# Kernel tuning notes

Hardware: AMD Instinct MI355X
Metric: run time of the kernel (lower is better)

The kernel has to match this reference:

```python
import jax, jax.numpy as jnp
import numpy as np

PAD, SOS, EOS = 0, 2, 3
B, S, T = 32, 64, 32
E, HE, HD = 300, 256, 512
VE, VD = 50000, 50000

def _p(k, shape, s=0.05):
    return jax.random.normal(k, shape, dtype=jnp.float32) * s

def setup_inputs():
    ks = jax.random.split(jax.random.key(0), 22)
    return dict(
        data=jax.random.randint(ks[0], (B, S), 0, VE),
        target=jax.random.randint(ks[1], (B, T), 0, VD),
        data_len=jnp.full((B,), S, dtype=jnp.int32),
        target_len=jnp.full((B,), T, dtype=jnp.int32),
        emb_enc=_p(ks[2], (VE, E)).at[PAD].set(0.0),
        emb_dec=_p(ks[3], (VD, E)).at[PAD].set(0.0),
        Wihf=_p(ks[4], (3 * HE, E)), Whhf=_p(ks[5], (3 * HE, HE)),
        bihf=_p(ks[6], (3 * HE,)), bhhf=_p(ks[7], (3 * HE,)),
        Wihb=_p(ks[8], (3 * HE, E)), Whhb=_p(ks[9], (3 * HE, HE)),
        bihb=_p(ks[10], (3 * HE,)), bhhb=_p(ks[11], (3 * HE,)),
        Wihd=_p(ks[12], (3 * HD, E + 2 * HE)), Whhd=_p(ks[13], (3 * HD, HD)),
        bihd=_p(ks[14], (3 * HD,)), bhhd=_p(ks[15], (3 * HD,)),
        Wattn=_p(ks[16], (2 * HE, HD + E)), battn=_p(ks[17], (2 * HE,)),
        Wout=_p(ks[18], (VD, HD)), bout=_p(ks[19], (VD,)),
    )

def gru_cell(x, h, W_ih, W_hh, b_ih, b_hh):
    # PyTorch GRU cell: gates ordered (r, z, n)
    gi = x @ W_ih.T + b_ih
    gh = h @ W_hh.T + b_hh
    i_r, i_z, i_n = jnp.split(gi, 3, axis=-1)
    h_r, h_z, h_n = jnp.split(gh, 3, axis=-1)
    r = jax.nn.sigmoid(i_r + h_r)
    z = jax.nn.sigmoid(i_z + h_z)
    n = jnp.tanh(i_n + r * h_n)
    return (1.0 - z) * n + z * h

def _forward(data, target, emb_enc, emb_dec, Wihf, Whhf, bihf, bhhf,
             Wihb, Whhb, bihb, bhhb, Wihd, Whhd, bihd, bhhd,
             Wattn, battn, Wout, bout):
    # ---- bidirectional 1-layer GRU encoder ----
    x = emb_enc[data]                          # [B,S,E] (dropout p=0 -> identity)
    xt = jnp.swapaxes(x, 0, 1)                 # [S,B,E]
    h0 = jnp.zeros((data.shape[0], HE), dtype=x.dtype)
    def stepf(h, xi):
        h2 = gru_cell(xi, h, Wihf, Whhf, bihf, bhhf)
        return h2, h2
    def stepb(h, xi):
        h2 = gru_cell(xi, h, Wihb, Whhb, bihb, bhhb)
        return h2, h2
    hf, yf = jax.lax.scan(stepf, h0, xt)
    hb, yb = jax.lax.scan(stepb, h0, xt[::-1])
    enc_out = jnp.swapaxes(jnp.concatenate([yf, yb[::-1]], axis=-1), 0, 1)  # [B,S,2HE]
    h_dec = jnp.concatenate([hf, hb], axis=-1)                              # [B,HD]

    # ---- greedy attention decoder loop (teacher_forcing_ratio=0.0) ----
    inp0 = jnp.full((data.shape[0],), SOS, dtype=jnp.int32)
    def dec_step(carry, _):
        h, inp = carry
        emb = emb_dec[inp]                                        # [B,E]
        q = jnp.concatenate([emb, h], axis=-1) @ Wattn.T + battn  # [B,2HE]
        scores = jnp.einsum('bd,bsd->bs', q, enc_out)             # [B,S]
        aw = jax.nn.softmax(scores, axis=-1)
        ctx = jnp.einsum('bs,bsd->bd', aw, enc_out)               # [B,2HE]
        h2 = gru_cell(jnp.concatenate([emb, ctx], axis=-1), h, Wihd, Whhd, bihd, bhhd)
        logp = jax.nn.log_softmax(h2 @ Wout.T + bout, axis=-1)    # [B,VD]
        nxt = jnp.argmax(logp, axis=-1).astype(jnp.int32)         # topk(1), detached
        return (h2, nxt), (logp, nxt, aw)
    _, (logps, idxs, aws) = jax.lax.scan(dec_step, (h_dec, inp0), None, length=T)
    decoder_output = jnp.swapaxes(logps, 0, 1)   # [B,T,VD]
    decoder_idx = jnp.swapaxes(idxs, 0, 1)       # [B,T]
    att_weights = jnp.swapaxes(aws, 0, 1)        # [B,T,S]
    # mask[i, j:] = 0 from the first EOS (inclusive)
    mask = (jnp.cumsum((decoder_idx == EOS).astype(jnp.int32), axis=1) == 0).astype(jnp.float32)
    return decoder_output, decoder_idx, mask, att_weights

def reference(data, target, data_len, target_len, emb_enc, emb_dec,
              Wihf, Whhf, bihf, bhhf, Wihb, Whhb, bihb, bhhb,
              Wihd, Whhd, bihd, bhhd, Wattn, battn, Wout, bout):
    return _forward(data, target, emb_enc, emb_dec, Wihf, Whhf, bihf, bhhf,
                    Wihb, Whhb, bihb, bhhb, Wihd, Whhd, bihd, bhhd,
                    Wattn, battn, Wout, bout)
```

## Files before the change

kernel.cpp:

```cpp
#include <hip/hip_runtime.h>
#include <stdint.h>

#define B 32
#define S 64
#define T 32
#define E 300
#define HE 256
#define HD 512
#define VD 50000
#define GE 768
#define GD 1536
#define CATN 812
#define SOS 2
#define EOS 3

#define SZ_WIHT3   (E*HE*3)
#define SZ_WHHT3   (HE*HE*3)
#define SZ_WATTNT4 (CATN*HD)
#define SZ_WIHDT3  (CATN*HD*3)
#define SZ_WHHDT3  (HD*HD*3)
#define SZ_GI      (S*B*HE*3)
#define SZ_ENCOUT  (B*S*HD)

constexpr size_t OFF_WIHT3F  = 0;
constexpr size_t OFF_WIHT3B  = OFF_WIHT3F + SZ_WIHT3 + 4;
constexpr size_t OFF_WHHT3F  = OFF_WIHT3B + SZ_WIHT3 + 4;
constexpr size_t OFF_WHHT3B  = OFF_WHHT3F + SZ_WHHT3 + 4;
constexpr size_t OFF_WATTNT4 = OFF_WHHT3B + SZ_WHHT3 + 4;
constexpr size_t OFF_WIHDT3  = OFF_WATTNT4 + SZ_WATTNT4;
constexpr size_t OFF_WHHDT3  = OFF_WIHDT3 + SZ_WIHDT3 + 4;
constexpr size_t OFF_GIF     = OFF_WHHDT3 + SZ_WHHDT3 + 4;
constexpr size_t OFF_GIB     = OFF_GIF + SZ_GI + 4;
constexpr size_t OFF_ENCOUT  = OFF_GIB + SZ_GI + 4;
constexpr size_t OFF_HBUF    = OFF_ENCOUT + SZ_ENCOUT;
constexpr size_t OFF_QBUF    = OFF_HBUF + B*HD;
constexpr size_t OFF_GHBUF   = OFF_QBUF + B*HD;
constexpr size_t OFF_GIEBUF  = OFF_GHBUF + 3*B*HD;
constexpr size_t OFF_CTXBUF  = OFF_GIEBUF + 3*B*HD;
constexpr size_t OFF_EXPSUM  = OFF_CTXBUF + B*HD;
constexpr size_t OFF_LSE     = OFF_EXPSUM + T*B;
constexpr size_t OFF_PACKED  = OFF_LSE + T*B;

constexpr size_t O_IDX  = (size_t)B*T*VD;
constexpr size_t O_MASK = O_IDX + B*T;
constexpr size_t O_ATT  = O_MASK + B*T;

struct __align__(4) f4u { float x, y, z, w; };
__device__ __forceinline__ f4u ld4u(const float* p) { return *(const f4u*)p; }

__device__ __forceinline__ float sigm(float x) { return 1.0f / (1.0f + __expf(-x)); }
__device__ __forceinline__ float tanhfast(float x) {
    float e = __expf(2.0f * fminf(x, 15.0f));
    return (e - 1.0f) / (e + 1.0f);
}

__global__ __launch_bounds__(256) void k_prep(
    const float* __restrict__ Wihf, const float* __restrict__ Whhf,
    const float* __restrict__ Wihb, const float* __restrict__ Whhb,
    const float* __restrict__ Wihd, const float* __restrict__ Whhd,
    const float* __restrict__ Wattn, float* __restrict__ ws)
{
    const size_t NWIH = (size_t)GE * E;
    const size_t NWHH = (size_t)GE * HE;
    const size_t NATT = (size_t)HD * CATN;
    const size_t NWID = (size_t)GD * CATN;
    const size_t NWHD = (size_t)GD * HD;
    size_t i = (size_t)blockIdx.x * 256 + threadIdx.x;

    if (i < 2 * NWIH) {
        int d = i >= NWIH;
        size_t r = i - (d ? NWIH : 0);
        int row = (int)(r / E), k = (int)(r - (size_t)row * E);
        int g = row >> 8, j = row & 255;
        const float* src = d ? Wihb : Wihf;
        ws[(d ? OFF_WIHT3B : OFF_WIHT3F) + ((size_t)k * HE + j) * 3 + g] = src[r];
        return;
    }
    i -= 2 * NWIH;
    if (i < 2 * NWHH) {
        int d = i >= NWHH;
        size_t r = i - (d ? NWHH : 0);
        int row = (int)(r / HE), k = (int)(r & (HE - 1));
        int g = row >> 8, j = row & 255;
        const float* src = d ? Whhb : Whhf;
        ws[(d ? OFF_WHHT3B : OFF_WHHT3F) + ((size_t)k * HE + j) * 3 + g] = src[r];
        return;
    }
    i -= 2 * NWHH;
    if (i < NATT) {
        int row = (int)(i / CATN), k = (int)(i - (size_t)row * CATN);
        ws[OFF_WATTNT4 + (((size_t)(k >> 2) * HD + row) << 2) + (k & 3)] = Wattn[i];
        return;
    }
    i -= NATT;
    if (i < NWID) {
        int row = (int)(i / CATN), k = (int)(i - (size_t)row * CATN);
        int g = row >> 9, j = row & 511;
        ws[OFF_WIHDT3 + ((size_t)k * HD + j) * 3 + g] = Wihd[i];
        return;
    }
    i -= NWID;
    if (i < NWHD) {
        int row = (int)(i / HD), k = (int)(i & (HD - 1));
        int g = row >> 9, j = row & 511;
        ws[OFF_WHHDT3 + ((size_t)k * HD + j) * 3 + g] = Whhd[i];
        return;
    }
    i -= NWHD;
    if (i < 4096) ws[OFF_EXPSUM + i] = 0.0f;
}

__global__ __launch_bounds__(256) void k_enc_gi(
    const int* __restrict__ data, const float* __restrict__ emb_enc,
    const float* __restrict__ bihf, const float* __restrict__ bihb,
    float* __restrict__ ws)
{
    int s = blockIdx.x, dir = blockIdx.y, b0 = blockIdx.z * 16;
    int tid = threadIdx.x;
    __shared__ float xT[E * 16];
    int s_eff = dir ? (S - 1 - s) : s;
    for (int idx = tid; idx < 16 * E; idx += 256) {
        int bb = idx / E, k = idx - bb * E;
        int tok = data[(b0 + bb) * S + s_eff];
        xT[k * 16 + bb] = emb_enc[(size_t)tok * E + k];
    }
    __syncthreads();
    const float* W3 = ws + (dir ? OFF_WIHT3B : OFF_WIHT3F);
    const float* bih = dir ? bihb : bihf;
    int j = tid;
    float aR[16], aZ[16], aN[16];
#pragma unroll
    for (int bb = 0; bb < 16; bb++) { aR[bb] = 0.f; aZ[bb] = 0.f; aN[bb] = 0.f; }
    for (int k = 0; k < E; k++) {
        f4u w = ld4u(W3 + ((size_t)k * HE + j) * 3);
        const float* xk = &xT[k * 16];
#pragma unroll
        for (int bb = 0; bb < 16; bb++) {
            float x = xk[bb];
            aR[bb] += x * w.x; aZ[bb] += x * w.y; aN[bb] += x * w.z;
        }
    }
    float br = bih[j], bz = bih[HE + j], bn = bih[2 * HE + j];
    float* gi = ws + (dir ? OFF_GIB : OFF_GIF);
#pragma unroll
    for (int bb = 0; bb < 16; bb++) {
        size_t base = (((size_t)s * B + b0 + bb) * HE + j) * 3;
        gi[base + 0] = aR[bb] + br;
        gi[base + 1] = aZ[bb] + bz;
        gi[base + 2] = aN[bb] + bn;
    }
}

__global__ __launch_bounds__(1024) void k_enc_rec(
    const float* __restrict__ bhhf, const float* __restrict__ bhhb,
    float* __restrict__ ws)
{
    int b = blockIdx.x, dir = blockIdx.y;
    int tid = threadIdx.x;
    int j = tid & 255, kc = tid >> 8;
    __shared__ float h[2][HE];
    __shared__ float part[3][4][HE];
    if (tid < HE) h[0][tid] = 0.f;
    __syncthreads();
    const float* W3 = ws + (dir ? OFF_WHHT3B : OFF_WHHT3F);
    const float* gi = ws + (dir ? OFF_GIB : OFF_GIF);
    const float* bhh = dir ? bhhb : bhhf;
    float* enc = ws + OFF_ENCOUT;
    float br = bhh[j], bz = bhh[HE + j], bn = bhh[2 * HE + j];
    const float* Wp = W3 + ((size_t)(kc * 64) * HE + j) * 3;
    for (int s = 0; s < S; s++) {
        const float* hc = h[s & 1];
        float gr = 0.f, gz = 0.f, gn = 0.f;
#pragma unroll 4
        for (int k4 = 0; k4 < 16; k4++) {
            float4 h4 = *(const float4*)&hc[kc * 64 + k4 * 4];
#pragma unroll
            for (int kk = 0; kk < 4; kk++) {
                f4u w = ld4u(Wp + ((size_t)(k4 * 4 + kk) * HE) * 3);
                float hv = (kk == 0) ? h4.x : (kk == 1) ? h4.y : (kk == 2) ? h4.z : h4.w;
                gr += hv * w.x; gz += hv * w.y; gn += hv * w.z;
            }
        }
        part[0][kc][j] = gr; part[1][kc][j] = gz; part[2][kc][j] = gn;
        __syncthreads();
        if (kc == 0) {
            float sgr = part[0][0][j] + part[0][1][j] + part[0][2][j] + part[0][3][j] + br;
            float sgz = part[1][0][j] + part[1][1][j] + part[1][2][j] + part[1][3][j] + bz;
            float sgn = part[2][0][j] + part[2][1][j] + part[2][2][j] + part[2][3][j] + bn;
            f4u g = ld4u(gi + (((size_t)s * B + b) * HE + j) * 3);
            float hold = hc[j];
            float r = sigm(g.x + sgr);
            float z = sigm(g.y + sgz);
            float n = tanhfast(g.z + r * sgn);
            float hn = (1.f - z) * n + z * hold;
            h[(s + 1) & 1][j] = hn;
            int s_store = dir ? (S - 1 - s) : s;
            enc[((size_t)b * S + s_store) * HD + dir * HE + j] = hn;
            if (s == S - 1) ws[OFF_HBUF + (size_t)b * HD + dir * HE + j] = hn;
        }
        __syncthreads();
    }
}

__device__ __forceinline__ int decode_inp(const float* ws, int t, int b) {
    if (t == 0) return SOS;
    const unsigned long long* pm = (const unsigned long long*)(ws + OFF_PACKED);
    unsigned long long p = pm[(size_t)(t - 1) * B + b];
    return (VD - 1) - (int)(unsigned)(p & 0xffffffffu);
}

__global__ __launch_bounds__(256) void k_dec1(
    const float* __restrict__ emb_dec, const float* __restrict__ battn,
    const float* __restrict__ bhhd, const float* __restrict__ bihd,
    float* __restrict__ ws, int t)
{
    int jc = blockIdx.x, bg = blockIdx.y, kind = blockIdx.z;
    int tid = threadIdx.x;
    int jl = tid & 31, bb8 = tid >> 5;
    int b0 = bg * 8;
    __shared__ float cat[8][816];
    for (int bb = 0; bb < 8; bb++) {
        int inp = decode_inp(ws, t, b0 + bb);
        const float* eb = emb_dec + (size_t)inp * E;
        const float* hb = ws + OFF_HBUF + (size_t)(b0 + bb) * HD;
        for (int k = tid; k < CATN; k += 256)
            cat[bb][k] = (k < E) ? eb[k] : hb[k - E];
    }
    __syncthreads();
    int j = jc * 32 + jl;
    int b = b0 + bb8;
    if (kind == 0) {
        float acc = battn[j];
        const float* W4 = ws + OFF_WATTNT4;
        for (int k4 = 0; k4 < CATN / 4; k4++) {
            float4 c4 = *(const float4*)&cat[bb8][k4 * 4];
            float4 w4 = *(const float4*)&W4[((size_t)k4 * HD + j) << 2];
            acc += c4.x * w4.x + c4.y * w4.y + c4.z * w4.z + c4.w * w4.w;
        }
        ws[OFF_QBUF + (size_t)b * HD + j] = acc;
    } else if (kind == 1) {
        float gr = bhhd[j], gz = bhhd[HD + j], gn = bhhd[2 * HD + j];
        const float* W3 = ws + OFF_WHHDT3;
        for (int k4 = 0; k4 < HD / 4; k4++) {
            float4 h4 = *(const float4*)&cat[bb8][E + k4 * 4];
#pragma unroll
            for (int kk = 0; kk < 4; kk++) {
                f4u w = ld4u(W3 + ((size_t)(k4 * 4 + kk) * HD + j) * 3);
                float hv = (kk == 0) ? h4.x : (kk == 1) ? h4.y : (kk == 2) ? h4.z : h4.w;
                gr += hv * w.x; gz += hv * w.y; gn += hv * w.z;
            }
        }
        float* gh = ws + OFF_GHBUF;
        gh[0 * B * HD + (size_t)b * HD + j] = gr;
        gh[1 * B * HD + (size_t)b * HD + j] = gz;
        gh[2 * B * HD + (size_t)b * HD + j] = gn;
    } else {
        float gr = bihd[j], gz = bihd[HD + j], gn = bihd[2 * HD + j];
        const float* W3 = ws + OFF_WIHDT3;
        for (int k4 = 0; k4 < E / 4; k4++) {
            float4 x4 = *(const float4*)&cat[bb8][k4 * 4];
#pragma unroll
            for (int kk = 0; kk < 4; kk++) {
                f4u w = ld4u(W3 + ((size_t)(k4 * 4 + kk) * HD + j) * 3);
                float xv = (kk == 0) ? x4.x : (kk == 1) ? x4.y : (kk == 2) ? x4.z : x4.w;
                gr += xv * w.x; gz += xv * w.y; gn += xv * w.z;
            }
        }
        float* ge = ws + OFF_GIEBUF;
        ge[0 * B * HD + (size_t)b * HD + j] = gr;
        ge[1 * B * HD + (size_t)b * HD + j] = gz;
        ge[2 * B * HD + (size_t)b * HD + j] = gn;
    }
}

__global__ __launch_bounds__(256) void k_dec_attn(
    float* __restrict__ ws, float* __restrict__ out, int t)
{
    int b = blockIdx.x, tid = threadIdx.x;
    __shared__ float q[HD];
    __shared__ float awl[S];
    const float* qb = ws + OFF_QBUF + (size_t)b * HD;
    for (int k = tid; k < HD; k += 256) q[k] = qb[k];
    __syncthreads();
    if (tid < S) {
        int s = tid;
        const float* enc = ws + OFF_ENCOUT + ((size_t)b * S + s) * HD;
        float sc = 0.f;
        for (int k4 = 0; k4 < HD / 4; k4++) {
            float4 q4 = *(const float4*)&q[k4 * 4];
            float4 e4 = *(const float4*)&enc[k4 * 4];
            sc += q4.x * e4.x + q4.y * e4.y + q4.z * e4.z + q4.w * e4.w;
        }
        float m = sc;
        for (int off = 32; off; off >>= 1) m = fmaxf(m, __shfl_xor(m, off));
        float e = __expf(sc - m);
        float sum = e;
        for (int off = 32; off; off >>= 1) sum += __shfl_xor(sum, off);
        float aw = e / sum;
        out[O_ATT + ((size_t)b * T + t) * S + s] = aw;
        awl[s] = aw;
    }
    __syncthreads();
    const float* encb = ws + OFF_ENCOUT + (size_t)b * S * HD;
    float* ctx = ws + OFF_CTXBUF + (size_t)b * HD;
    for (int jj = 0; jj < HD / 256; jj++) {
        int jIdx = jj * 256 + tid;
        float acc = 0.f;
        for (int ss = 0; ss < S; ss++) acc += awl[ss] * encb[(size_t)ss * HD + jIdx];
        ctx[jIdx] = acc;
    }
}

__global__ __launch_bounds__(256) void k_dec3(float* __restrict__ ws, int t)
{
    int jc = blockIdx.x, bg = blockIdx.y;
    int tid = threadIdx.x;
    int jl = tid & 31, bb = tid >> 5;
    int j = jc * 32 + jl, b = bg * 8 + bb;
    __shared__ float xc[8 * HD];
    for (int idx = tid; idx < 8 * HD; idx += 256) {
        int bbb = idx >> 9, k = idx & 511;
        xc[idx] = ws[OFF_CTXBUF + (size_t)(bg * 8 + bbb) * HD + k];
    }
    __syncthreads();
    const float* W3 = ws + OFF_WIHDT3;
    float gr = ws[OFF_GIEBUF + 0 * B * HD + (size_t)b * HD + j];
    float gz = ws[OFF_GIEBUF + 1 * B * HD + (size_t)b * HD + j];
    float gn = ws[OFF_GIEBUF + 2 * B * HD + (size_t)b * HD + j];
    const float* xrow = &xc[bb * HD];
    for (int k4 = 0; k4 < HD / 4; k4++) {
        float4 x4 = *(const float4*)&xrow[k4 * 4];
#pragma unroll
        for (int kk = 0; kk < 4; kk++) {
            f4u w = ld4u(W3 + ((size_t)(E + k4 * 4 + kk) * HD + j) * 3);
            float xv = (kk == 0) ? x4.x : (kk == 1) ? x4.y : (kk == 2) ? x4.z : x4.w;
            gr += xv * w.x; gz += xv * w.y; gn += xv * w.z;
        }
    }
    float ghr = ws[OFF_GHBUF + 0 * B * HD + (size_t)b * HD + j];
    float ghz = ws[OFF_GHBUF + 1 * B * HD + (size_t)b * HD + j];
    float ghn = ws[OFF_GHBUF + 2 * B * HD + (size_t)b * HD + j];
    float hold = ws[OFF_HBUF + (size_t)b * HD + j];
    float r = sigm(gr + ghr);
    float z = sigm(gz + ghz);
    float n = tanhfast(gn + r * ghn);
    ws[OFF_HBUF + (size_t)b * HD + j] = (1.f - z) * n + z * hold;
}

__global__ __launch_bounds__(256) void k_proj(
    const float* __restrict__ Wout, const float* __restrict__ bout,
    float* __restrict__ ws, float* __restrict__ out, int t)
{
    int v = blockIdx.x * 256 + threadIdx.x;
    int b0 = blockIdx.y * 8;
    bool valid = v < VD;
    __shared__ float hl[8 * HD];
    __shared__ float red_e[4][8];
    __shared__ unsigned long long red_m[4][8];
    const float* hb = ws + OFF_HBUF;
    for (int idx = threadIdx.x; idx < 8 * HD; idx += 256)
        hl[idx] = hb[(size_t)(b0 + (idx >> 9)) * HD + (idx & 511)];
    __syncthreads();

    float acc[8];
    float bo = valid ? bout[v] : 0.f;
#pragma unroll
    for (int bb = 0; bb < 8; bb++) acc[bb] = bo;
    const float* wrow = Wout + (size_t)(valid ? v : 0) * HD;
    for (int k4 = 0; k4 < HD / 4; k4++) {
        float4 w4 = *(const float4*)&wrow[k4 * 4];
#pragma unroll
        for (int bb = 0; bb < 8; bb++) {
            float4 h4 = *(const float4*)&hl[bb * HD + k4 * 4];
            acc[bb] = fmaf(w4.x, h4.x, fmaf(w4.y, h4.y,
                      fmaf(w4.z, h4.z, fmaf(w4.w, h4.w, acc[bb]))));
        }
    }
    if (valid) {
#pragma unroll
        for (int bb = 0; bb < 8; bb++)
            out[((size_t)(b0 + bb) * T + t) * VD + v] = acc[bb];
    }
    int wv = threadIdx.x >> 6, lane = threadIdx.x & 63;
#pragma unroll
    for (int bb = 0; bb < 8; bb++) {
        float val = valid ? acc[bb] : -__builtin_inff();
        unsigned u = __float_as_uint(val);
        u = (u & 0x80000000u) ? ~u : (u | 0x80000000u);
        unsigned long long pk =
            ((unsigned long long)u << 32) | (unsigned)(valid ? (VD - 1 - v) : 0);
        float e = valid ? __expf(acc[bb]) : 0.f;
        for (int off = 32; off; off >>= 1) {
            unsigned long long o = __shfl_xor(pk, off);
            pk = (o > pk) ? o : pk;
            e += __shfl_xor(e, off);
        }
        if (lane == 0) { red_e[wv][bb] = e; red_m[wv][bb] = pk; }
    }
    __syncthreads();
    if (threadIdx.x < 8) {
        int bb = threadIdx.x;
        float e = red_e[0][bb] + red_e[1][bb] + red_e[2][bb] + red_e[3][bb];
        unsigned long long pk = red_m[0][bb];
        pk = red_m[1][bb] > pk ? red_m[1][bb] : pk;
        pk = red_m[2][bb] > pk ? red_m[2][bb] : pk;
        pk = red_m[3][bb] > pk ? red_m[3][bb] : pk;
        atomicAdd(ws + OFF_EXPSUM + (size_t)t * B + b0 + bb, e);
        atomicMax((unsigned long long*)(ws + OFF_PACKED) + (size_t)t * B + b0 + bb, pk);
    }
}

__global__ void k_fin_small(float* __restrict__ ws, float* __restrict__ out)
{
    int b = threadIdx.x;
    if (b >= B) return;
    const unsigned long long* pmax = (const unsigned long long*)(ws + OFF_PACKED);
    int eos = 0;
    for (int t = 0; t < T; t++) {
        unsigned long long p = pmax[(size_t)t * B + b];
        int v = (VD - 1) - (int)(unsigned)(p & 0xffffffffu);
        out[O_IDX + (size_t)b * T + t] = (float)v;
        if (v == EOS) eos++;
        out[O_MASK + (size_t)b * T + t] = (eos == 0) ? 1.f : 0.f;
        ws[OFF_LSE + (size_t)t * B + b] = logf(ws[OFF_EXPSUM + (size_t)t * B + b]);
    }
}

__global__ __launch_bounds__(256) void k_logp(
    const float* __restrict__ ws, float* __restrict__ out)
{
    size_t gid = (size_t)blockIdx.x * 256 + threadIdx.x;
    const size_t NQ = (size_t)B * T * (VD / 4);
    if (gid >= NQ) return;
    size_t row = gid / (VD / 4);
    int c4 = (int)(gid - row * (VD / 4));
    int b = (int)(row >> 5), t = (int)(row & 31);
    float L = ws[OFF_LSE + (size_t)t * B + b];
    float4* p = (float4*)(out + row * VD + (size_t)c4 * 4);
    float4 x = *p;
    x.x -= L; x.y -= L; x.z -= L; x.w -= L;
    *p = x;
}

extern "C" void kernel_launch(void* const* d_in, const int* in_sizes, int n_in,
                              void* d_out, int out_size, void* d_ws, size_t ws_size,
                              hipStream_t stream)
{
    (void)in_sizes; (void)n_in; (void)out_size; (void)ws_size;
    const int*   data    = (const int*)d_in[0];
    const float* emb_enc = (const float*)d_in[4];
    const float* emb_dec = (const float*)d_in[5];
    const float* Wihf    = (const float*)d_in[6];
    const float* Whhf    = (const float*)d_in[7];
    const float* bihf    = (const float*)d_in[8];
    const float* bhhf    = (const float*)d_in[9];
    const float* Wihb    = (const float*)d_in[10];
    const float* Whhb    = (const float*)d_in[11];
    const float* bihb    = (const float*)d_in[12];
    const float* bhhb    = (const float*)d_in[13];
    const float* Wihd    = (const float*)d_in[14];
    const float* Whhd    = (const float*)d_in[15];
    const float* bihd    = (const float*)d_in[16];
    const float* bhhd    = (const float*)d_in[17];
    const float* Wattn   = (const float*)d_in[18];
    const float* battn   = (const float*)d_in[19];
    const float* Wout    = (const float*)d_in[20];
    const float* bout    = (const float*)d_in[21];
    float* ws  = (float*)d_ws;
    float* out = (float*)d_out;

    k_prep<<<dim3(12920), dim3(256), 0, stream>>>(Wihf, Whhf, Wihb, Whhb,
                                                  Wihd, Whhd, Wattn, ws);
    k_enc_gi<<<dim3(S, 2, 2), dim3(256), 0, stream>>>(data, emb_enc, bihf, bihb, ws);
    k_enc_rec<<<dim3(B, 2), dim3(1024), 0, stream>>>(bhhf, bhhb, ws);

    for (int t = 0; t < T; t++) {
        k_dec1<<<dim3(16, 4, 3), dim3(256), 0, stream>>>(emb_dec, battn, bhhd, bihd, ws, t);
        k_dec_attn<<<dim3(B), dim3(256), 0, stream>>>(ws, out, t);
        k_dec3<<<dim3(16, 4), dim3(256), 0, stream>>>(ws, t);
        k_proj<<<dim3((VD + 255) / 256, 4), dim3(256), 0, stream>>>(Wout, bout, ws, out, t);
    }
    k_fin_small<<<dim3(1), dim3(64), 0, stream>>>(ws, out);
    k_logp<<<dim3((B * T * (VD / 4) + 255) / 256), dim3(256), 0, stream>>>(ws, out);
}
```

Before: 7.998 ms.

## Transpose Wout for coalesced projection, batch encoder recurrence, fuse decoder GRU kernels

Adds a one-time transpose of Wout into the workspace so the per-step vocabulary projection reads coalesced columns, and widens each projection block to 16 batch rows so every weight read is reused more. The encoder recurrence now processes 4 batch rows per block, reusing each weight load across them. The decoder's three-way kernel and the context GRU kernel are restructured into a query kernel and one fused GRU kernel, with a double-buffered hidden state. Attention scores move to a wave-parallel dot product. The cost is an extra transpose pass and workspace for a 100MB copy of Wout, plus higher register pressure in the projection.

```diff
diff --git a/kernel.cpp b/kernel.cpp
--- a/kernel.cpp
+++ b/kernel.cpp
@@ -33,13 +33,12 @@
 constexpr size_t OFF_GIB     = OFF_GIF + SZ_GI + 4;
 constexpr size_t OFF_ENCOUT  = OFF_GIB + SZ_GI + 4;
 constexpr size_t OFF_HBUF    = OFF_ENCOUT + SZ_ENCOUT;
-constexpr size_t OFF_QBUF    = OFF_HBUF + B*HD;
-constexpr size_t OFF_GHBUF   = OFF_QBUF + B*HD;
-constexpr size_t OFF_GIEBUF  = OFF_GHBUF + 3*B*HD;
-constexpr size_t OFF_CTXBUF  = OFF_GIEBUF + 3*B*HD;
+constexpr size_t OFF_QBUF    = OFF_HBUF + 2*B*HD;
+constexpr size_t OFF_CTXBUF  = OFF_QBUF + B*HD;
 constexpr size_t OFF_EXPSUM  = OFF_CTXBUF + B*HD;
 constexpr size_t OFF_LSE     = OFF_EXPSUM + T*B;
 constexpr size_t OFF_PACKED  = OFF_LSE + T*B;
+constexpr size_t OFF_WOUTT   = OFF_PACKED + 2*T*B;
 
 constexpr size_t O_IDX  = (size_t)B*T*VD;
 constexpr size_t O_MASK = O_IDX + B*T;
@@ -110,6 +109,28 @@
     if (i < 4096) ws[OFF_EXPSUM + i] = 0.0f;
 }
 
+__global__ __launch_bounds__(256) void k_transp(
+    const float* __restrict__ Wout, float* __restrict__ ws)
+{
+    __shared__ float tile[64][65];
+    int k0 = blockIdx.x * 64, v0 = blockIdx.y * 64;
+    int c = threadIdx.x & 63, r0 = threadIdx.x >> 6;
+#pragma unroll
+    for (int rr = 0; rr < 16; rr++) {
+        int r = r0 * 16 + rr;
+        int v = v0 + r;
+        tile[r][c] = (v < VD) ? Wout[(size_t)v * HD + k0 + c] : 0.f;
+    }
+    __syncthreads();
+    float* WT = ws + OFF_WOUTT;
+#pragma unroll
+    for (int rr = 0; rr < 16; rr++) {
+        int r = r0 * 16 + rr;
+        int v = v0 + c;
+        if (v < VD) WT[(size_t)(k0 + r) * VD + v] = tile[c][r];
+    }
+}
+
 __global__ __launch_bounds__(256) void k_enc_gi(
     const int* __restrict__ data, const float* __restrict__ emb_enc,
     const float* __restrict__ bihf, const float* __restrict__ bihb,
@@ -155,12 +176,12 @@
     const float* __restrict__ bhhf, const float* __restrict__ bhhb,
     float* __restrict__ ws)
 {
-    int b = blockIdx.x, dir = blockIdx.y;
+    int b0 = blockIdx.x * 4, dir = blockIdx.y;
     int tid = threadIdx.x;
     int j = tid & 255, kc = tid >> 8;
-    __shared__ float h[2][HE];
-    __shared__ float part[3][4][HE];
-    if (tid < HE) h[0][tid] = 0.f;
+    __shared__ float h[2][4][HE];
+    __shared__ float part[4][4][3][HE];
+    h[0][tid >> 8][tid & 255] = 0.f;
     __syncthreads();
     const float* W3 = ws + (dir ? OFF_WHHT3B : OFF_WHHT3F);
     const float* gi = ws + (dir ? OFF_GIB : OFF_GIF);
@@ -169,34 +190,49 @@
     float br = bhh[j], bz = bhh[HE + j], bn = bhh[2 * HE + j];
     const float* Wp = W3 + ((size_t)(kc * 64) * HE + j) * 3;
     for (int s = 0; s < S; s++) {
-        const float* hc = h[s & 1];
-        float gr = 0.f, gz = 0.f, gn = 0.f;
-#pragma unroll 4
+        int cur = s & 1, nxt = cur ^ 1;
+        float ar[4], az[4], an[4];
+#pragma unroll
+        for (int bb = 0; bb < 4; bb++) { ar[bb] = 0.f; az[bb] = 0.f; an[bb] = 0.f; }
+#pragma unroll 2
         for (int k4 = 0; k4 < 16; k4++) {
-            float4 h4 = *(const float4*)&hc[kc * 64 + k4 * 4];
+            float4 h4[4];
+#pragma unroll
+            for (int bb = 0; bb < 4; bb++)
+                h4[bb] = *(const float4*)&h[cur][bb][kc * 64 + k4 * 4];
 #pragma unroll
             for (int kk = 0; kk < 4; kk++) {
                 f4u w = ld4u(Wp + ((size_t)(k4 * 4 + kk) * HE) * 3);
-                float hv = (kk == 0) ? h4.x : (kk == 1) ? h4.y : (kk == 2) ? h4.z : h4.w;
-                gr += hv * w.x; gz += hv * w.y; gn += hv * w.z;
+#pragma unroll
+                for (int bb = 0; bb < 4; bb++) {
+                    float hv = (kk == 0) ? h4[bb].x : (kk == 1) ? h4[bb].y
+                             : (kk == 2) ? h4[bb].z : h4[bb].w;
+                    ar[bb] += hv * w.x; az[bb] += hv * w.y; an[bb] += hv * w.z;
+                }
             }
         }
-        part[0][kc][j] = gr; part[1][kc][j] = gz; part[2][kc][j] = gn;
+#pragma unroll
+        for (int bb = 0; bb < 4; bb++) {
+            part[kc][bb][0][j] = ar[bb];
+            part[kc][bb][1][j] = az[bb];
+            part[kc][bb][2][j] = an[bb];
+        }
         __syncthreads();
-        if (kc == 0) {
-            float sgr = part[0][0][j] + part[0][1][j] + part[0][2][j] + part[0][3][j] + br;
-            float sgz = part[1][0][j] + part[1][1][j] + part[1][2][j] + part[1][3][j] + bz;
-            float sgn = part[2][0][j] + part[2][1][j] + part[2][2][j] + part[2][3][j] + bn;
-            f4u g = ld4u(gi + (((size_t)s * B + b) * HE + j) * 3);
-            float hold = hc[j];
+        {
+            int bb = kc;
+            float sgr = part[0][bb][0][j] + part[1][bb][0][j] + part[2][bb][0][j] + part[3][bb][0][j] + br;
+            float sgz = part[0][bb][1][j] + part[1][bb][1][j] + part[2][bb][1][j] + part[3][bb][1][j] + bz;
+            float sgn = part[0][bb][2][j] + part[1][bb][2][j] + part[2][bb][2][j] + part[3][bb][2][j] + bn;
+            f4u g = ld4u(gi + (((size_t)s * B + b0 + bb) * HE + j) * 3);
+            float hold = h[cur][bb][j];
             float r = sigm(g.x + sgr);
             float z = sigm(g.y + sgz);
             float n = tanhfast(g.z + r * sgn);
             float hn = (1.f - z) * n + z * hold;
-            h[(s + 1) & 1][j] = hn;
+            h[nxt][bb][j] = hn;
             int s_store = dir ? (S - 1 - s) : s;
-            enc[((size_t)b * S + s_store) * HD + dir * HE + j] = hn;
-            if (s == S - 1) ws[OFF_HBUF + (size_t)b * HD + dir * HE + j] = hn;
+            enc[((size_t)(b0 + bb) * S + s_store) * HD + dir * HE + j] = hn;
+            if (s == S - 1) ws[OFF_HBUF + (size_t)(b0 + bb) * HD + dir * HE + j] = hn;
         }
         __syncthreads();
     }
@@ -209,181 +245,181 @@
     return (VD - 1) - (int)(unsigned)(p & 0xffffffffu);
 }
 
-__global__ __launch_bounds__(256) void k_dec1(
+__global__ __launch_bounds__(256) void k_dq(
     const float* __restrict__ emb_dec, const float* __restrict__ battn,
-    const float* __restrict__ bhhd, const float* __restrict__ bihd,
     float* __restrict__ ws, int t)
 {
-    int jc = blockIdx.x, bg = blockIdx.y, kind = blockIdx.z;
+    int jc = blockIdx.x, b0 = blockIdx.y * 8;
     int tid = threadIdx.x;
     int jl = tid & 31, bb8 = tid >> 5;
-    int b0 = bg * 8;
+    const float* hcur = ws + OFF_HBUF + (size_t)(t & 1) * B * HD;
     __shared__ float cat[8][816];
     for (int bb = 0; bb < 8; bb++) {
         int inp = decode_inp(ws, t, b0 + bb);
         const float* eb = emb_dec + (size_t)inp * E;
-        const float* hb = ws + OFF_HBUF + (size_t)(b0 + bb) * HD;
+        const float* hb = hcur + (size_t)(b0 + bb) * HD;
         for (int k = tid; k < CATN; k += 256)
             cat[bb][k] = (k < E) ? eb[k] : hb[k - E];
     }
     __syncthreads();
-    int j = jc * 32 + jl;
-    int b = b0 + bb8;
-    if (kind == 0) {
-        float acc = battn[j];
-        const float* W4 = ws + OFF_WATTNT4;
-        for (int k4 = 0; k4 < CATN / 4; k4++) {
-            float4 c4 = *(const float4*)&cat[bb8][k4 * 4];
-            float4 w4 = *(const float4*)&W4[((size_t)k4 * HD + j) << 2];
-            acc += c4.x * w4.x + c4.y * w4.y + c4.z * w4.z + c4.w * w4.w;
-        }
-        ws[OFF_QBUF + (size_t)b * HD + j] = acc;
-    } else if (kind == 1) {
-        float gr = bhhd[j], gz = bhhd[HD + j], gn = bhhd[2 * HD + j];
-        const float* W3 = ws + OFF_WHHDT3;
-        for (int k4 = 0; k4 < HD / 4; k4++) {
-            float4 h4 = *(const float4*)&cat[bb8][E + k4 * 4];
-#pragma unroll
-            for (int kk = 0; kk < 4; kk++) {
-                f4u w = ld4u(W3 + ((size_t)(k4 * 4 + kk) * HD + j) * 3);
-                float hv = (kk == 0) ? h4.x : (kk == 1) ? h4.y : (kk == 2) ? h4.z : h4.w;
-                gr += hv * w.x; gz += hv * w.y; gn += hv * w.z;
-            }
-        }
-        float* gh = ws + OFF_GHBUF;
-        gh[0 * B * HD + (size_t)b * HD + j] = gr;
-        gh[1 * B * HD + (size_t)b * HD + j] = gz;
-        gh[2 * B * HD + (size_t)b * HD + j] = gn;
-    } else {
-        float gr = bihd[j], gz = bihd[HD + j], gn = bihd[2 * HD + j];
-        const float* W3 = ws + OFF_WIHDT3;
-        for (int k4 = 0; k4 < E / 4; k4++) {
-            float4 x4 = *(const float4*)&cat[bb8][k4 * 4];
-#pragma unroll
-            for (int kk = 0; kk < 4; kk++) {
-                f4u w = ld4u(W3 + ((size_t)(k4 * 4 + kk) * HD + j) * 3);
-                float xv = (kk == 0) ? x4.x : (kk == 1) ? x4.y : (kk == 2) ? x4.z : x4.w;
-                gr += xv * w.x; gz += xv * w.y; gn += xv * w.z;
-            }
-        }
-        float* ge = ws + OFF_GIEBUF;
-        ge[0 * B * HD + (size_t)b * HD + j] = gr;
-        ge[1 * B * HD + (size_t)b * HD + j] = gz;
-        ge[2 * B * HD + (size_t)b * HD + j] = gn;
-    }
-}
-
-__global__ __launch_bounds__(256) void k_dec_attn(
+    int j = jc * 32 + jl, b = b0 + bb8;
+    float acc = battn[j];
+    const float* W4 = ws + OFF_WATTNT4;
+    for (int k4 = 0; k4 < CATN / 4; k4++) {
+        float4 c4 = *(const float4*)&cat[bb8][k4 * 4];
+        float4 w4 = *(const float4*)&W4[((size_t)k4 * HD + j) << 2];
+        acc += c4.x * w4.x + c4.y * w4.y + c4.z * w4.z + c4.w * w4.w;
+    }
+    ws[OFF_QBUF + (size_t)b * HD + j] = acc;
+}
+
+__global__ __launch_bounds__(256) void k_attn(
     float* __restrict__ ws, float* __restrict__ out, int t)
 {
     int b = blockIdx.x, tid = threadIdx.x;
+    int wv = tid >> 6, lane = tid & 63;
     __shared__ float q[HD];
+    __shared__ float scs[S];
     __shared__ float awl[S];
     const float* qb = ws + OFF_QBUF + (size_t)b * HD;
     for (int k = tid; k < HD; k += 256) q[k] = qb[k];
     __syncthreads();
-    if (tid < S) {
-        int s = tid;
-        const float* enc = ws + OFF_ENCOUT + ((size_t)b * S + s) * HD;
-        float sc = 0.f;
-        for (int k4 = 0; k4 < HD / 4; k4++) {
-            float4 q4 = *(const float4*)&q[k4 * 4];
-            float4 e4 = *(const float4*)&enc[k4 * 4];
-            sc += q4.x * e4.x + q4.y * e4.y + q4.z * e4.z + q4.w * e4.w;
-        }
-        float m = sc;
+    const float* encb = ws + OFF_ENCOUT + (size_t)b * S * HD;
+    float4 qa = *(const float4*)&q[lane * 4];
+    float4 qb4 = *(const float4*)&q[256 + lane * 4];
+#pragma unroll 4
+    for (int i = 0; i < 16; i++) {
+        int s = wv * 16 + i;
+        const float* e = encb + (size_t)s * HD;
+        float4 ea = *(const float4*)&e[lane * 4];
+        float4 eb = *(const float4*)&e[256 + lane * 4];
+        float p = ea.x * qa.x + ea.y * qa.y + ea.z * qa.z + ea.w * qa.w
+                + eb.x * qb4.x + eb.y * qb4.y + eb.z * qb4.z + eb.w * qb4.w;
+        for (int off = 32; off; off >>= 1) p += __shfl_xor(p, off);
+        if (lane == 0) scs[s] = p;
+    }
+    __syncthreads();
+    if (tid < 64) {
+        float v = scs[tid];
+        float m = v;
         for (int off = 32; off; off >>= 1) m = fmaxf(m, __shfl_xor(m, off));
-        float e = __expf(sc - m);
+        float e = __expf(v - m);
         float sum = e;
         for (int off = 32; off; off >>= 1) sum += __shfl_xor(sum, off);
         float aw = e / sum;
-        out[O_ATT + ((size_t)b * T + t) * S + s] = aw;
-        awl[s] = aw;
-    }
-    __syncthreads();
-    const float* encb = ws + OFF_ENCOUT + (size_t)b * S * HD;
+        awl[tid] = aw;
+        out[O_ATT + ((size_t)b * T + t) * S + tid] = aw;
+    }
+    __syncthreads();
     float* ctx = ws + OFF_CTXBUF + (size_t)b * HD;
-    for (int jj = 0; jj < HD / 256; jj++) {
-        int jIdx = jj * 256 + tid;
+    for (int j = tid; j < HD; j += 256) {
         float acc = 0.f;
-        for (int ss = 0; ss < S; ss++) acc += awl[ss] * encb[(size_t)ss * HD + jIdx];
-        ctx[jIdx] = acc;
-    }
-}
-
-__global__ __launch_bounds__(256) void k_dec3(float* __restrict__ ws, int t)
-{
-    int jc = blockIdx.x, bg = blockIdx.y;
+        for (int ss = 0; ss < S; ss++) acc += awl[ss] * encb[(size_t)ss * HD + j];
+        ctx[j] = acc;
+    }
+}
+
+__global__ __launch_bounds__(256) void k_dgru(
+    const float* __restrict__ emb_dec,
+    const float* __restrict__ bihd, const float* __restrict__ bhhd,
+    float* __restrict__ ws, int t)
+{
+    int jc = blockIdx.x, b0 = blockIdx.y * 8;
     int tid = threadIdx.x;
-    int jl = tid & 31, bb = tid >> 5;
-    int j = jc * 32 + jl, b = bg * 8 + bb;
-    __shared__ float xc[8 * HD];
-    for (int idx = tid; idx < 8 * HD; idx += 256) {
-        int bbb = idx >> 9, k = idx & 511;
-        xc[idx] = ws[OFF_CTXBUF + (size_t)(bg * 8 + bbb) * HD + k];
-    }
-    __syncthreads();
-    const float* W3 = ws + OFF_WIHDT3;
-    float gr = ws[OFF_GIEBUF + 0 * B * HD + (size_t)b * HD + j];
-    float gz = ws[OFF_GIEBUF + 1 * B * HD + (size_t)b * HD + j];
-    float gn = ws[OFF_GIEBUF + 2 * B * HD + (size_t)b * HD + j];
-    const float* xrow = &xc[bb * HD];
-    for (int k4 = 0; k4 < HD / 4; k4++) {
-        float4 x4 = *(const float4*)&xrow[k4 * 4];
+    int jl = tid & 31, bb8 = tid >> 5;
+    const float* hcur = ws + OFF_HBUF + (size_t)(t & 1) * B * HD;
+    float* hnxt = ws + OFF_HBUF + (size_t)((t + 1) & 1) * B * HD;
+    __shared__ float se[8][300];
+    __shared__ float sh[8][512];
+    __shared__ float sc[8][512];
+    for (int bb = 0; bb < 8; bb++) {
+        int inp = decode_inp(ws, t, b0 + bb);
+        const float* eb = emb_dec + (size_t)inp * E;
+        const float* hb = hcur + (size_t)(b0 + bb) * HD;
+        const float* cx = ws + OFF_CTXBUF + (size_t)(b0 + bb) * HD;
+        for (int k = tid; k < E; k += 256) se[bb][k] = eb[k];
+        for (int k = tid; k < HD; k += 256) { sh[bb][k] = hb[k]; sc[bb][k] = cx[k]; }
+    }
+    __syncthreads();
+    int j = jc * 32 + jl, b = b0 + bb8;
+    float gr = bihd[j], gz = bihd[HD + j], gn = bihd[2 * HD + j];
+    const float* W3i = ws + OFF_WIHDT3;
+    for (int k4 = 0; k4 < E / 4; k4++) {
+        float4 x4 = *(const float4*)&se[bb8][k4 * 4];
 #pragma unroll
         for (int kk = 0; kk < 4; kk++) {
-            f4u w = ld4u(W3 + ((size_t)(E + k4 * 4 + kk) * HD + j) * 3);
+            f4u w = ld4u(W3i + ((size_t)(k4 * 4 + kk) * HD + j) * 3);
             float xv = (kk == 0) ? x4.x : (kk == 1) ? x4.y : (kk == 2) ? x4.z : x4.w;
             gr += xv * w.x; gz += xv * w.y; gn += xv * w.z;
         }
     }
-    float ghr = ws[OFF_GHBUF + 0 * B * HD + (size_t)b * HD + j];
-    float ghz = ws[OFF_GHBUF + 1 * B * HD + (size_t)b * HD + j];
-    float ghn = ws[OFF_GHBUF + 2 * B * HD + (size_t)b * HD + j];
-    float hold = ws[OFF_HBUF + (size_t)b * HD + j];
-    float r = sigm(gr + ghr);
-    float z = sigm(gz + ghz);
-    float n = tanhfast(gn + r * ghn);
-    ws[OFF_HBUF + (size_t)b * HD + j] = (1.f - z) * n + z * hold;
+    for (int k4 = 0; k4 < HD / 4; k4++) {
+        float4 x4 = *(const float4*)&sc[bb8][k4 * 4];
+#pragma unroll
+        for (int kk = 0; kk < 4; kk++) {
+            f4u w = ld4u(W3i + ((size_t)(E + k4 * 4 + kk) * HD + j) * 3);
+            float xv = (kk == 0) ? x4.x : (kk == 1) ? x4.y : (kk == 2) ? x4.z : x4.w;
+            gr += xv * w.x; gz += xv * w.y; gn += xv * w.z;
+        }
+    }
+    float hr = bhhd[j], hz = bhhd[HD + j], hn_ = bhhd[2 * HD + j];
+    const float* W3h = ws + OFF_WHHDT3;
+    for (int k4 = 0; k4 < HD / 4; k4++) {
+        float4 x4 = *(const float4*)&sh[bb8][k4 * 4];
+#pragma unroll
+        for (int kk = 0; kk < 4; kk++) {
+            f4u w = ld4u(W3h + ((size_t)(k4 * 4 + kk) * HD + j) * 3);
+            float xv = (kk == 0) ? x4.x : (kk == 1) ? x4.y : (kk == 2) ? x4.z : x4.w;
+            hr += xv * w.x; hz += xv * w.y; hn_ += xv * w.z;
+        }
+    }
+    float hold = sh[bb8][j];
+    float r = sigm(gr + hr);
+    float z = sigm(gz + hz);
+    float n = tanhfast(gn + r * hn_);
+    hnxt[(size_t)b * HD + j] = (1.f - z) * n + z * hold;
 }
 
 __global__ __launch_bounds__(256) void k_proj(
-    const float* __restrict__ Wout, const float* __restrict__ bout,
+    const float* __restrict__ bout,
     float* __restrict__ ws, float* __restrict__ out, int t)
 {
     int v = blockIdx.x * 256 + threadIdx.x;
-    int b0 = blockIdx.y * 8;
+    int b0 = blockIdx.y * 16;
     bool valid = v < VD;
-    __shared__ float hl[8 * HD];
-    __shared__ float red_e[4][8];
-    __shared__ unsigned long long red_m[4][8];
-    const float* hb = ws + OFF_HBUF;
-    for (int idx = threadIdx.x; idx < 8 * HD; idx += 256)
-        hl[idx] = hb[(size_t)(b0 + (idx >> 9)) * HD + (idx & 511)];
-    __syncthreads();
-
-    float acc[8];
-    float bo = valid ? bout[v] : 0.f;
-#pragma unroll
-    for (int bb = 0; bb < 8; bb++) acc[bb] = bo;
-    const float* wrow = Wout + (size_t)(valid ? v : 0) * HD;
+    int vc = valid ? v : (VD - 1);
+    __shared__ float hl[16 * 512];
+    __shared__ float red_e[4][16];
+    __shared__ unsigned long long red_m[4][16];
+    const float* hsrc = ws + OFF_HBUF + (size_t)((t + 1) & 1) * B * HD + (size_t)b0 * HD;
+    for (int idx = threadIdx.x; idx < 16 * 512; idx += 256) hl[idx] = hsrc[idx];
+    __syncthreads();
+
+    float acc[16];
+    float bo = bout[vc];
+#pragma unroll
+    for (int bb = 0; bb < 16; bb++) acc[bb] = bo;
+    const float* WT = ws + OFF_WOUTT;
     for (int k4 = 0; k4 < HD / 4; k4++) {
-        float4 w4 = *(const float4*)&wrow[k4 * 4];
-#pragma unroll
-        for (int bb = 0; bb < 8; bb++) {
-            float4 h4 = *(const float4*)&hl[bb * HD + k4 * 4];
-            acc[bb] = fmaf(w4.x, h4.x, fmaf(w4.y, h4.y,
-                      fmaf(w4.z, h4.z, fmaf(w4.w, h4.w, acc[bb]))));
+        float w0 = WT[(size_t)(k4 * 4 + 0) * VD + vc];
+        float w1 = WT[(size_t)(k4 * 4 + 1) * VD + vc];
+        float w2 = WT[(size_t)(k4 * 4 + 2) * VD + vc];
+        float w3 = WT[(size_t)(k4 * 4 + 3) * VD + vc];
+#pragma unroll
+        for (int bb = 0; bb < 16; bb++) {
+            float4 h4 = *(const float4*)&hl[bb * 512 + k4 * 4];
+            acc[bb] = fmaf(w0, h4.x, fmaf(w1, h4.y,
+                      fmaf(w2, h4.z, fmaf(w3, h4.w, acc[bb]))));
         }
     }
     if (valid) {
 #pragma unroll
-        for (int bb = 0; bb < 8; bb++)
+        for (int bb = 0; bb < 16; bb++)
             out[((size_t)(b0 + bb) * T + t) * VD + v] = acc[bb];
     }
     int wv = threadIdx.x >> 6, lane = threadIdx.x & 63;
 #pragma unroll
-    for (int bb = 0; bb < 8; bb++) {
+    for (int bb = 0; bb < 16; bb++) {
         float val = valid ? acc[bb] : -__builtin_inff();
         unsigned u = __float_as_uint(val);
         u = (u & 0x80000000u) ? ~u : (u | 0x80000000u);
@@ -398,7 +434,7 @@
         if (lane == 0) { red_e[wv][bb] = e; red_m[wv][bb] = pk; }
     }
     __syncthreads();
-    if (threadIdx.x < 8) {
+    if (threadIdx.x < 16) {
         int bb = threadIdx.x;
         float e = red_e[0][bb] + red_e[1][bb] + red_e[2][bb] + red_e[3][bb];
         unsigned long long pk = red_m[0][bb];
@@ -471,14 +507,15 @@
 
     k_prep<<<dim3(12920), dim3(256), 0, stream>>>(Wihf, Whhf, Wihb, Whhb,
                                                   Wihd, Whhd, Wattn, ws);
+    k_transp<<<dim3(HD / 64, (VD + 63) / 64), dim3(256), 0, stream>>>(Wout, ws);
     k_enc_gi<<<dim3(S, 2, 2), dim3(256), 0, stream>>>(data, emb_enc, bihf, bihb, ws);
-    k_enc_rec<<<dim3(B, 2), dim3(1024), 0, stream>>>(bhhf, bhhb, ws);
+    k_enc_rec<<<dim3(8, 2), dim3(1024), 0, stream>>>(bhhf, bhhb, ws);
 
     for (int t = 0; t < T; t++) {
-        k_dec1<<<dim3(16, 4, 3), dim3(256), 0, stream>>>(emb_dec, battn, bhhd, bihd, ws, t);
-        k_dec_attn<<<dim3(B), dim3(256), 0, stream>>>(ws, out, t);
-        k_dec3<<<dim3(16, 4), dim3(256), 0, stream>>>(ws, t);
-        k_proj<<<dim3((VD + 255) / 256, 4), dim3(256), 0, stream>>>(Wout, bout, ws, out, t);
+        k_dq<<<dim3(16, 4), dim3(256), 0, stream>>>(emb_dec, battn, ws, t);
+        k_attn<<<dim3(B), dim3(256), 0, stream>>>(ws, out, t);
+        k_dgru<<<dim3(16, 4), dim3(256), 0, stream>>>(emb_dec, bihd, bhhd, ws, t);
+        k_proj<<<dim3(196, 2), dim3(256), 0, stream>>>(bout, ws, out, t);
     }
     k_fin_small<<<dim3(1), dim3(64), 0, stream>>>(ws, out);
     k_logp<<<dim3((B * T * (VD / 4) + 255) / 256), dim3(256), 0, stream>>>(ws, out);
```

After: 9.083 ms. 13.6% more time.
